# Performance work log

Measured on AMD Instinct MI355X. Metric: run time of the kernel, lower is better.

The kernel has to match this reference:

```python
import jax, jax.numpy as jnp
import numpy as np

N = 100_000      # nodes
E = 1_600_000    # edges
F_IN = 4         # num_features
H = 128          # hidden_channels
C = 5            # num_classes
G = 256          # graphs in batch


def setup_inputs() -> dict:
    key = jax.random.key(0)
    ks = jax.random.split(key, 14)
    x = jax.random.normal(ks[0], (N, F_IN), dtype=jnp.float32)
    edge_index = jax.random.randint(ks[1], (2, E), 0, N, dtype=jnp.int64)
    batch = jnp.sort(jax.random.randint(ks[2], (N,), 0, G, dtype=jnp.int64))
    def lin(k, fan_in, fan_out):
        kw, kb = jax.random.split(k)
        s = 1.0 / np.sqrt(fan_in)
        W = jax.random.uniform(kw, (fan_in, fan_out), jnp.float32, -s, s)
        b = jax.random.uniform(kb, (fan_out,), jnp.float32, -s, s)
        return W, b
    W1, b1 = lin(ks[3], F_IN, H)
    W2, b2 = lin(ks[4], H, H)
    W3, b3 = lin(ks[5], H, H)
    W4, b4 = lin(ks[6], H, H)
    Wl, bl = lin(ks[7], H, C)
    return {"x": x, "edge_index": edge_index, "batch": batch,
            "W1": W1, "b1": b1, "W2": W2, "b2": b2,
            "W3": W3, "b3": b3, "W4": W4, "b4": b4,
            "Wl": Wl, "bl": bl}


def reference(x, edge_index, batch, W1, b1, W2, b2, W3, b3, W4, b4, Wl, bl):
    n = x.shape[0]
    loop = jnp.arange(n, dtype=edge_index.dtype)
    src = jnp.concatenate([edge_index[0], loop])  # [E+N], with self-loops
    dst = jnp.concatenate([edge_index[1], loop])
    # symmetric normalization on A + I (PyG GCNConv default)
    deg = jax.ops.segment_sum(jnp.ones_like(dst, dtype=x.dtype), dst, num_segments=n)
    dinv = deg ** -0.5  # deg >= 1 thanks to self-loops
    coef = dinv[src] * dinv[dst]  # per-edge norm [E+N]

    def conv(h, W, b):
        h = h @ W                               # [N, H]
        msg = h[src] * coef[:, None]            # gather + scale [E+N, H]
        return jax.ops.segment_sum(msg, dst, num_segments=n) + b

    h = jax.nn.relu(conv(x, W1, b1))
    h = jax.nn.relu(conv(h, W2, b2))
    h = jax.nn.relu(conv(h, W3, b3))
    h = jax.nn.relu(conv(h, W4, b4))

    # global_mean_pool over graph ids
    counts = jax.ops.segment_sum(jnp.ones((n,), h.dtype), batch, num_segments=G)
    pooled = jax.ops.segment_sum(h, batch, num_segments=G)
    pooled = pooled / jnp.maximum(counts, 1.0)[:, None]  # [G, H]

    return jax.nn.sigmoid(pooled @ Wl + bl)  # [G, C]
```

## Files before the change

kernel.cpp:

```cpp
#include <hip/hip_runtime.h>
#include <hip/hip_fp8.h>
#include <math.h>

#define N_NODES 100000
#define N_EDGES 1600000
#define F_IN    4
#define HID     128
#define N_CLS   5
#define N_GRAPH 256
#define POOL_SEG 8

#define BSHIFT   9
#define BSIZE    512
#define NBUK     196
#define NCHUNK   200
#define CHUNK    8000

typedef _Float16 f16;
typedef _Float16 f16x2 __attribute__((ext_vector_type(2)));
typedef _Float16 f16x8 __attribute__((ext_vector_type(8)));
typedef float f32x4 __attribute__((ext_vector_type(4)));

__device__ __forceinline__ float rec_coef(unsigned r) {
    return (float)__builtin_bit_cast(_Float16, (unsigned short)(r & 0x7FFFu));
}

__device__ __forceinline__ float2 fp8x2_to_f32x2(unsigned short raw) {
    __hip_fp8x2_e4m3 t;
    t.__x = raw;
    return static_cast<float2>(t);
}

__device__ __forceinline__ void fma8(float c, uint2 v, float* acc) {
    float2 p0 = fp8x2_to_f32x2((unsigned short)(v.x & 0xFFFFu));
    float2 p1 = fp8x2_to_f32x2((unsigned short)(v.x >> 16));
    float2 p2 = fp8x2_to_f32x2((unsigned short)(v.y & 0xFFFFu));
    float2 p3 = fp8x2_to_f32x2((unsigned short)(v.y >> 16));
    acc[0] = fmaf(c, p0.x, acc[0]); acc[1] = fmaf(c, p0.y, acc[1]);
    acc[2] = fmaf(c, p1.x, acc[2]); acc[3] = fmaf(c, p1.y, acc[3]);
    acc[4] = fmaf(c, p2.x, acc[4]); acc[5] = fmaf(c, p2.y, acc[5]);
    acc[6] = fmaf(c, p3.x, acc[6]); acc[7] = fmaf(c, p3.y, acc[7]);
}

__global__ __launch_bounds__(256) void k_bc(const int* __restrict__ dst, int* __restrict__ C) {
    __shared__ int cnt[NBUK];
    int t = threadIdx.x;
    if (t < NBUK) cnt[t] = 0;
    __syncthreads();
    int base = blockIdx.x * CHUNK;
#pragma unroll
    for (int it = 0; it < 32; ++it) {
        int idx = it * 256 + t;
        if (idx < CHUNK) atomicAdd(&cnt[dst[base + idx] >> BSHIFT], 1);
    }
    __syncthreads();
    if (t < NBUK) C[blockIdx.x * NBUK + t] = cnt[t];
}

__global__ __launch_bounds__(256) void k_bscan(const int* __restrict__ C, int* __restrict__ Off,
                                               int* __restrict__ bbase) {
    __shared__ int s[256];
    int b = threadIdx.x;
    int tot = 0;
    if (b < NBUK) {
        for (int c = 0; c < NCHUNK; ++c) {
            Off[c * NBUK + b] = tot;
            tot += C[c * NBUK + b];
        }
    }
    s[b] = (b < NBUK) ? tot : 0;
    __syncthreads();
    for (int off = 1; off < 256; off <<= 1) {
        int v = (b >= off) ? s[b - off] : 0;
        __syncthreads();
        s[b] += v;
        __syncthreads();
    }
    if (b < NBUK) bbase[b] = s[b] - tot;
    if (b == 0) bbase[NBUK] = N_EDGES;
}

__global__ __launch_bounds__(256) void k_scatter(const int* __restrict__ src, const int* __restrict__ dst,
                                                 const int* __restrict__ Off, const int* __restrict__ bbase,
                                                 unsigned* __restrict__ bkt) {
    __shared__ int cur[NBUK];
    int t = threadIdx.x;
    if (t < NBUK) cur[t] = bbase[t] + Off[blockIdx.x * NBUK + t];
    __syncthreads();
    int base = blockIdx.x * CHUNK;
#pragma unroll
    for (int it = 0; it < 32; ++it) {
        int idx = it * 256 + t;
        if (idx < CHUNK) {
            int s = src[base + idx], d = dst[base + idx];
            int b = d >> BSHIFT;
            int p = atomicAdd(&cur[b], 1);
            bkt[p] = ((unsigned)s << BSHIFT) | (unsigned)(d & (BSIZE - 1));
        }
    }
}

__global__ __launch_bounds__(256) void k_hist2(const unsigned* __restrict__ bkt,
                                               const int* __restrict__ bbase,
                                               int* __restrict__ deg, float* __restrict__ dinv,
                                               int* __restrict__ padTot) {
    __shared__ int hist[BSIZE];
    __shared__ int tot;
    int t = threadIdx.x, b = blockIdx.x;
    hist[t] = 0; hist[t + 256] = 0;
    if (t == 0) tot = 0;
    __syncthreads();
    int s0 = bbase[b], s1 = bbase[b + 1];
    for (int e = s0 + t; e < s1; e += 256) atomicAdd(&hist[bkt[e] & (BSIZE - 1)], 1);
    __syncthreads();
    int loc = 0;
#pragma unroll
    for (int h = 0; h < 2; ++h) {
        int l = t + h * 256;
        int node = b * BSIZE + l;
        int d = hist[l];
        if (node < N_NODES) {
            deg[node] = d;
            dinv[node] = rsqrtf((float)d + 1.0f);
        }
        loc += (d + 15) >> 4;
    }
    atomicAdd(&tot, loc);
    __syncthreads();
    if (t == 0) padTot[b] = tot << 4;
}

__global__ __launch_bounds__(256) void k_pscan(const int* __restrict__ padTot, int* __restrict__ padBase,
                                               int* __restrict__ rowptrP) {
    __shared__ int s[256];
    int b = threadIdx.x;
    int v = (b < NBUK) ? padTot[b] : 0;
    s[b] = v;
    __syncthreads();
    for (int off = 1; off < 256; off <<= 1) {
        int u = (b >= off) ? s[b - off] : 0;
        __syncthreads();
        s[b] += u;
        __syncthreads();
    }
    if (b < NBUK) padBase[b] = s[b] - v;
    if (b == 0) {
        padBase[NBUK] = s[NBUK - 1];
        rowptrP[N_NODES] = s[NBUK - 1];
    }
}

__global__ __launch_bounds__(256) void k_local2(const unsigned* __restrict__ bkt,
                                                const int* __restrict__ bbase,
                                                const int* __restrict__ deg,
                                                const float* __restrict__ dinv,
                                                const int* __restrict__ padBase,
                                                int* __restrict__ rowptrP,
                                                unsigned* __restrict__ edges) {
    __shared__ int sc[BSIZE];
    __shared__ int cur[BSIZE];
    __shared__ float dv[BSIZE];
    int t = threadIdx.x, b = blockIdx.x;
    int base = padBase[b];
    int n0 = b * BSIZE + t, n1 = n0 + 256;
    int d0 = (n0 < N_NODES) ? deg[n0] : 0;
    int d1 = (n1 < N_NODES) ? deg[n1] : 0;
    int p0 = ((d0 + 15) >> 4) << 4;
    int p1 = ((d1 + 15) >> 4) << 4;
    sc[t] = p0; sc[t + 256] = p1;
    dv[t] = (n0 < N_NODES) ? dinv[n0] : 0.f;
    dv[t + 256] = (n1 < N_NODES) ? dinv[n1] : 0.f;
    __syncthreads();
    for (int off = 1; off < BSIZE; off <<= 1) {
        int i0 = t, i1 = t + 256;
        int v0 = (i0 >= off) ? sc[i0 - off] : 0;
        int v1 = (i1 >= off) ? sc[i1 - off] : 0;
        __syncthreads();
        sc[i0] += v0; sc[i1] += v1;
        __syncthreads();
    }
    int off0 = base + sc[t] - p0;
    int off1 = base + sc[t + 256] - p1;
    if (n0 < N_NODES) rowptrP[n0] = off0;
    if (n1 < N_NODES) rowptrP[n1] = off1;
    cur[t] = off0; cur[t + 256] = off1;
    int padT = sc[BSIZE - 1];
    for (int i = base + t; i < base + padT; i += 256) edges[i] = 0;
    __syncthreads();
    int s0 = bbase[b], s1 = bbase[b + 1];
    for (int e = s0 + t; e < s1; e += 256) {
        unsigned r = bkt[e];
        int dl = (int)(r & (BSIZE - 1));
        int s = (int)(r >> BSHIFT);
        int p = atomicAdd(&cur[dl], 1);
        float c = dv[dl] * dinv[s];
        unsigned short cb = __builtin_bit_cast(unsigned short, (f16)c);
        edges[p] = ((unsigned)s << 15) | (unsigned)(cb & 0x7FFFu);
    }
}

__global__ __launch_bounds__(256) void k_aggx1(const float4* __restrict__ x,
                                               const int* __restrict__ rowptrP,
                                               const unsigned* __restrict__ edges,
                                               const float* __restrict__ dinv,
                                               const float* __restrict__ W1, const float* __restrict__ b1,
                                               unsigned* __restrict__ hA) {
    __shared__ float4 sxa[16];
    __shared__ float sW[4 * HID];
    __shared__ float sb[HID];
    int t = threadIdx.x;
    sW[t] = W1[t];
    sW[t + 256] = W1[t + 256];
    if (t < HID) sb[t] = b1[t];
    int grp = t >> 4;
    int l = t & 15;
    int node = blockIdx.x * 16 + grp;
    int beg = rowptrP[node], end = rowptrP[node + 1];
    float ax = 0.f, ay = 0.f, az = 0.f, aw = 0.f;
    for (int e = beg + l; e < end; e += 16) {
        unsigned r = edges[e];
        float c = rec_coef(r);
        float4 v = x[r >> 15];
        ax = fmaf(c, v.x, ax); ay = fmaf(c, v.y, ay);
        az = fmaf(c, v.z, az); aw = fmaf(c, v.w, aw);
    }
#pragma unroll
    for (int off = 1; off < 16; off <<= 1) {
        ax += __shfl_xor(ax, off, 64);
        ay += __shfl_xor(ay, off, 64);
        az += __shfl_xor(az, off, 64);
        aw += __shfl_xor(aw, off, 64);
    }
    if (l == 0) {
        float di = dinv[node];
        float c0 = di * di;
        float4 xv = x[node];
        sxa[grp] = make_float4(fmaf(c0, xv.x, ax), fmaf(c0, xv.y, ay),
                               fmaf(c0, xv.z, az), fmaf(c0, xv.w, aw));
    }
    __syncthreads();

    int node0 = blockIdx.x * 16;
#pragma unroll
    for (int it = 0; it < 2; ++it) {
        int id = it * 256 + t;
        int n = id >> 5;
        int g = id & 31;
        float4 a = sxa[n];
        float c[4];
#pragma unroll
        for (int j = 0; j < 4; ++j) {
            int col = g * 4 + j;
            float v = sb[col];
            v = fmaf(a.x, sW[col],           v);
            v = fmaf(a.y, sW[HID + col],     v);
            v = fmaf(a.z, sW[2 * HID + col], v);
            v = fmaf(a.w, sW[3 * HID + col], v);
            c[j] = fmaxf(v, 0.0f);
        }
        unsigned lo = __hip_fp8x2_e4m3(make_float2(c[0], c[1])).__x;
        unsigned hi = __hip_fp8x2_e4m3(make_float2(c[2], c[3])).__x;
        hA[(node0 + n) * 32 + g] = lo | (hi << 16);
    }
}

template <bool FP8OUT>
__global__ __launch_bounds__(1024, 8) void k_aggemm8(const unsigned* __restrict__ h8,
                                                     const int* __restrict__ rowptrP,
                                                     const unsigned* __restrict__ edges,
                                                     const float* __restrict__ dinv,
                                                     const f16* __restrict__ Wp,
                                                     const float* __restrict__ bias,
                                                     void* __restrict__ outv) {
    __shared__ f16 S[16 * HID];
    int wave = threadIdx.x >> 6;
    int lane = threadIdx.x & 63;
    int node0 = blockIdx.x * 16;
    int node = node0 + wave;
    int g = lane >> 4;
    int l = lane & 15;
    int beg = rowptrP[node], end = rowptrP[node + 1];
    const char* hp = (const char*)h8 + l * 8;

    float acc[8];
    {
        float di = dinv[node];
        float c0 = (g == 0) ? di * di : 0.0f;
        uint2 v = *(const uint2*)(hp + ((size_t)node << 7));
        float2 p0 = fp8x2_to_f32x2((unsigned short)(v.x & 0xFFFFu));
        float2 p1 = fp8x2_to_f32x2((unsigned short)(v.x >> 16));
        float2 p2 = fp8x2_to_f32x2((unsigned short)(v.y & 0xFFFFu));
        float2 p3 = fp8x2_to_f32x2((unsigned short)(v.y >> 16));
        acc[0] = c0 * p0.x; acc[1] = c0 * p0.y;
        acc[2] = c0 * p1.x; acc[3] = c0 * p1.y;
        acc[4] = c0 * p2.x; acc[5] = c0 * p2.y;
        acc[6] = c0 * p3.x; acc[7] = c0 * p3.y;
    }

    for (int e = beg; e < end; e += 16) {
        unsigned rec16 = edges[e + l];
#pragma unroll
        for (int i = 0; i < 4; ++i) {
            unsigned rec = __shfl(rec16, i * 4 + g, 64);
            float c = rec_coef(rec);
            uint2 v = *(const uint2*)(hp + ((rec >> 8) & 0xFFFFFF80u));
            fma8(c, v, acc);
        }
    }

#pragma unroll
    for (int j = 0; j < 8; ++j) {
        acc[j] += __shfl_xor(acc[j], 16, 64);
        acc[j] += __shfl_xor(acc[j], 32, 64);
    }
    if (lane < 16) {
        f16x8 o;
#pragma unroll
        for (int j = 0; j < 8; ++j) o[j] = (f16)acc[j];
        int dw = (l * 4) ^ ((wave & 7) << 2);
        *(f16x8*)&S[wave * HID + dw * 2] = o;
    }
    __syncthreads();

    if (wave < 8) {
        int t = wave;
        int m = lane & 15;
        int q = lane >> 4;
        f32x4 c4 = (f32x4){0.f, 0.f, 0.f, 0.f};
#pragma unroll
        for (int ks = 0; ks < 4; ++ks) {
            int dw = (ks * 16 + q * 4) ^ ((m & 7) << 2);
            f16x8 a = *(const f16x8*)&S[m * HID + dw * 2];
            f16x8 b = *(const f16x8*)(Wp + ((size_t)(t * 4 + ks) * 64 + lane) * 8);
            c4 = __builtin_amdgcn_mfma_f32_16x16x32_f16(a, b, c4, 0, 0, 0);
        }
        float bb = bias[t * 16 + m];
#pragma unroll
        for (int r = 0; r < 4; ++r) {
            float val = fmaxf(c4[r] + bb, 0.0f);
            int row = node0 + q * 4 + r;
            if constexpr (FP8OUT) {
                ((__hip_fp8_e4m3*)outv)[(size_t)row * HID + t * 16 + m] = __hip_fp8_e4m3(val);
            } else {
                ((f16*)outv)[(size_t)row * HID + t * 16 + m] = (f16)val;
            }
        }
    }
}

__global__ __launch_bounds__(256) void k_packW3(const float* __restrict__ W2, const float* __restrict__ W3,
                                                const float* __restrict__ W4, f16* __restrict__ Wp) {
    int idx = blockIdx.x * 256 + threadIdx.x;
    int which = idx >> 14;
    int r = idx & 16383;
    const float* W = (which == 0) ? W2 : (which == 1) ? W3 : W4;
    int j  = r & 7;
    int L  = (r >> 3) & 63;
    int ks = (r >> 9) & 3;
    int ct = r >> 11;
    int k = ks * 32 + (L >> 4) * 8 + j;
    int n = ct * 16 + (L & 15);
    Wp[idx] = (f16)W[k * HID + n];
}

__device__ __forceinline__ int lower_bound_batch(const int* __restrict__ batch, int val) {
    int lo = 0, hi = N_NODES;
    while (lo < hi) { int m = (lo + hi) >> 1; if (batch[m] < val) lo = m + 1; else hi = m; }
    return lo;
}

__global__ __launch_bounds__(128) void k_pool1(const f16* __restrict__ h, const int* __restrict__ batch,
                                               float* __restrict__ partials) {
    int g = blockIdx.x / POOL_SEG;
    int s = blockIdx.x % POOL_SEG;
    int f = threadIdx.x;
    int beg = lower_bound_batch(batch, g);
    int end = lower_bound_batch(batch, g + 1);
    int len = end - beg;
    int sb = beg + (int)(((long long)len * s) / POOL_SEG);
    int se = beg + (int)(((long long)len * (s + 1)) / POOL_SEG);
    float acc = 0.0f;
    for (int i = sb; i < se; ++i) acc += (float)h[i * HID + f];
    partials[(size_t)blockIdx.x * HID + f] = acc;
}

__global__ __launch_bounds__(128) void k_pool2h(const float* __restrict__ partials,
                                                const int* __restrict__ batch,
                                                const float* __restrict__ Wl, const float* __restrict__ bl,
                                                float* __restrict__ out) {
    __shared__ float sp[HID];
    int g = blockIdx.x;
    int f = threadIdx.x;
    float acc = 0.0f;
#pragma unroll
    for (int s = 0; s < POOL_SEG; ++s)
        acc += partials[(size_t)(g * POOL_SEG + s) * HID + f];
    int beg = lower_bound_batch(batch, g);
    int end = lower_bound_batch(batch, g + 1);
    sp[f] = acc / fmaxf((float)(end - beg), 1.0f);
    __syncthreads();
    if (f < N_CLS) {
        float v = bl[f];
        for (int k = 0; k < HID; ++k) v = fmaf(sp[k], Wl[k * N_CLS + f], v);
        out[g * N_CLS + f] = 1.0f / (1.0f + expf(-v));
    }
}

extern "C" void kernel_launch(void* const* d_in, const int* in_sizes, int n_in,
                              void* d_out, int out_size, void* d_ws, size_t ws_size,
                              hipStream_t stream) {
    const float* x     = (const float*)d_in[0];
    const int*   ei    = (const int*)d_in[1];
    const int*   batch = (const int*)d_in[2];
    const float* W1 = (const float*)d_in[3];  const float* b1 = (const float*)d_in[4];
    const float* W2 = (const float*)d_in[5];  const float* b2 = (const float*)d_in[6];
    const float* W3 = (const float*)d_in[7];  const float* b3 = (const float*)d_in[8];
    const float* W4 = (const float*)d_in[9];  const float* b4 = (const float*)d_in[10];
    const float* Wl = (const float*)d_in[11]; const float* bl = (const float*)d_in[12];
    float* out = (float*)d_out;

    const size_t EPAD = (size_t)N_EDGES + (size_t)N_NODES * 16;

    char* p = (char*)d_ws;
    auto alloc = [&](size_t bytes) { char* r = p; p += (bytes + 255) & ~(size_t)255; return (void*)r; };
    int*      C       = (int*)     alloc((size_t)NCHUNK * NBUK * 4);
    int*      Off     = (int*)     alloc((size_t)NCHUNK * NBUK * 4);
    int*      bbase   = (int*)     alloc((size_t)(NBUK + 1) * 4);
    int*      padTot  = (int*)     alloc((size_t)NBUK * 4);
    int*      padBase = (int*)     alloc((size_t)(NBUK + 1) * 4);
    unsigned* bkt     = (unsigned*)alloc((size_t)N_EDGES * 4);
    int*      deg     = (int*)     alloc((size_t)N_NODES * 4);
    int*      rowptrP = (int*)     alloc((size_t)(N_NODES + 1) * 4);
    float*    dinv    = (float*)   alloc((size_t)N_NODES * 4);
    unsigned* edges   = (unsigned*)alloc(EPAD * 4);
    unsigned* hA      = (unsigned*)alloc((size_t)N_NODES * HID);
    unsigned* hC      = (unsigned*)alloc((size_t)N_NODES * HID);
    f16*      h4      = (f16*)     alloc((size_t)N_NODES * HID * 2);
    float*    parts   = (float*)   alloc((size_t)N_GRAPH * POOL_SEG * HID * 4);
    f16*      Wp      = (f16*)     alloc((size_t)3 * HID * HID * 2);
    f16*      Wp2 = Wp;
    f16*      Wp3 = Wp + HID * HID;
    f16*      Wp4 = Wp + 2 * HID * HID;

    const int* srcv = ei;
    const int* dstv = ei + N_EDGES;

    k_bc     <<<NCHUNK, 256, 0, stream>>>(dstv, C);
    k_bscan  <<<1, 256, 0, stream>>>(C, Off, bbase);
    k_scatter<<<NCHUNK, 256, 0, stream>>>(srcv, dstv, Off, bbase, bkt);
    k_hist2  <<<NBUK, 256, 0, stream>>>(bkt, bbase, deg, dinv, padTot);
    k_pscan  <<<1, 256, 0, stream>>>(padTot, padBase, rowptrP);
    k_local2 <<<NBUK, 256, 0, stream>>>(bkt, bbase, deg, dinv, padBase, rowptrP, edges);

    k_packW3<<<192, 256, 0, stream>>>(W2, W3, W4, Wp);

    k_aggx1<<<N_NODES / 16, 256, 0, stream>>>((const float4*)x, rowptrP, edges, dinv, W1, b1, hA);

    const int fgrid = N_NODES / 16;
    k_aggemm8<true ><<<fgrid, 1024, 0, stream>>>(hA, rowptrP, edges, dinv, Wp2, b2, hC);
    k_aggemm8<true ><<<fgrid, 1024, 0, stream>>>(hC, rowptrP, edges, dinv, Wp3, b3, hA);
    k_aggemm8<false><<<fgrid, 1024, 0, stream>>>(hA, rowptrP, edges, dinv, Wp4, b4, h4);

    k_pool1 <<<N_GRAPH * POOL_SEG, 128, 0, stream>>>(h4, batch, parts);
    k_pool2h<<<N_GRAPH, 128, 0, stream>>>(parts, batch, Wl, bl, out);
}
```

Before: 359.1 us.

## Use packed fp16 accumulation and 4-edge padding in fp8 aggregation kernel

The gather-aggregate kernel now accumulates in packed f16x2 using a direct fp8-to-f16 conversion builtin, halving accumulator registers and FMA count. Per-node edge padding shrinks from 16 to 4, so less padded work is done. Edge records are loaded directly per lane group with guarded loads instead of a shuffle. Row bounds are made wave-uniform with readfirstlane. Accumulating in fp16 risks precision loss on high-degree nodes, and the guarded loads add branches.

Measured after the change: 382.3 us. 6.5% more time.

```diff
diff --git a/kernel.cpp b/kernel.cpp
--- a/kernel.cpp
+++ b/kernel.cpp
@@ -25,21 +25,39 @@
     return (float)__builtin_bit_cast(_Float16, (unsigned short)(r & 0x7FFFu));
 }
 
+__device__ __forceinline__ f16x2 rec_coef2(unsigned r) {
+    unsigned c = r & 0x7FFFu;
+    return __builtin_bit_cast(f16x2, (c << 16) | c);
+}
+
 __device__ __forceinline__ float2 fp8x2_to_f32x2(unsigned short raw) {
     __hip_fp8x2_e4m3 t;
     t.__x = raw;
     return static_cast<float2>(t);
 }
 
-__device__ __forceinline__ void fma8(float c, uint2 v, float* acc) {
-    float2 p0 = fp8x2_to_f32x2((unsigned short)(v.x & 0xFFFFu));
-    float2 p1 = fp8x2_to_f32x2((unsigned short)(v.x >> 16));
-    float2 p2 = fp8x2_to_f32x2((unsigned short)(v.y & 0xFFFFu));
-    float2 p3 = fp8x2_to_f32x2((unsigned short)(v.y >> 16));
-    acc[0] = fmaf(c, p0.x, acc[0]); acc[1] = fmaf(c, p0.y, acc[1]);
-    acc[2] = fmaf(c, p1.x, acc[2]); acc[3] = fmaf(c, p1.y, acc[3]);
-    acc[4] = fmaf(c, p2.x, acc[4]); acc[5] = fmaf(c, p2.y, acc[5]);
-    acc[6] = fmaf(c, p3.x, acc[6]); acc[7] = fmaf(c, p3.y, acc[7]);
+#if __has_builtin(__builtin_amdgcn_cvt_pk_f16_fp8)
+__device__ __forceinline__ f16x2 cvt_h2(unsigned v) {
+    auto t = __builtin_amdgcn_cvt_pk_f16_fp8((short)v);
+    return __builtin_bit_cast(f16x2, t);
+}
+#else
+__device__ __forceinline__ f16x2 cvt_h2(unsigned v) {
+    float2 f = fp8x2_to_f32x2((unsigned short)v);
+    auto t = __builtin_amdgcn_cvt_pkrtz(f.x, f.y);
+    return __builtin_bit_cast(f16x2, t);
+}
+#endif
+
+__device__ __forceinline__ void fma8h(f16x2 c2, uint2 v, f16x2* acc) {
+    acc[0] += c2 * cvt_h2(v.x);
+    acc[1] += c2 * cvt_h2(v.x >> 16);
+    acc[2] += c2 * cvt_h2(v.y);
+    acc[3] += c2 * cvt_h2(v.y >> 16);
+}
+
+__device__ __forceinline__ f16x2 shfl_xor_h2(f16x2 a, int m) {
+    return __builtin_bit_cast(f16x2, __shfl_xor(__builtin_bit_cast(int, a), m, 64));
 }
 
 __global__ __launch_bounds__(256) void k_bc(const int* __restrict__ dst, int* __restrict__ C) {
@@ -123,11 +141,11 @@
             deg[node] = d;
             dinv[node] = rsqrtf((float)d + 1.0f);
         }
-        loc += (d + 15) >> 4;
+        loc += (d + 3) >> 2;
     }
     atomicAdd(&tot, loc);
     __syncthreads();
-    if (t == 0) padTot[b] = tot << 4;
+    if (t == 0) padTot[b] = tot << 2;
 }
 
 __global__ __launch_bounds__(256) void k_pscan(const int* __restrict__ padTot, int* __restrict__ padBase,
@@ -165,8 +183,8 @@
     int n0 = b * BSIZE + t, n1 = n0 + 256;
     int d0 = (n0 < N_NODES) ? deg[n0] : 0;
     int d1 = (n1 < N_NODES) ? deg[n1] : 0;
-    int p0 = ((d0 + 15) >> 4) << 4;
-    int p1 = ((d1 + 15) >> 4) << 4;
+    int p0 = ((d0 + 3) >> 2) << 2;
+    int p1 = ((d1 + 3) >> 2) << 2;
     sc[t] = p0; sc[t + 256] = p1;
     dv[t] = (n0 < N_NODES) ? dinv[n0] : 0.f;
     dv[t + 256] = (n1 < N_NODES) ? dinv[n1] : 0.f;
@@ -279,44 +297,47 @@
     int node = node0 + wave;
     int g = lane >> 4;
     int l = lane & 15;
-    int beg = rowptrP[node], end = rowptrP[node + 1];
-    const char* hp = (const char*)h8 + l * 8;
-
-    float acc[8];
+    int beg = __builtin_amdgcn_readfirstlane(rowptrP[node]);
+    int end = __builtin_amdgcn_readfirstlane(rowptrP[node + 1]);
+    const char* h8c = (const char*)h8;
+    unsigned lo8 = (unsigned)(l * 8);
+
+    f16x2 acc[4];
+    acc[0] = (f16x2){0, 0}; acc[1] = (f16x2){0, 0};
+    acc[2] = (f16x2){0, 0}; acc[3] = (f16x2){0, 0};
     {
         float di = dinv[node];
-        float c0 = (g == 0) ? di * di : 0.0f;
-        uint2 v = *(const uint2*)(hp + ((size_t)node << 7));
-        float2 p0 = fp8x2_to_f32x2((unsigned short)(v.x & 0xFFFFu));
-        float2 p1 = fp8x2_to_f32x2((unsigned short)(v.x >> 16));
-        float2 p2 = fp8x2_to_f32x2((unsigned short)(v.y & 0xFFFFu));
-        float2 p3 = fp8x2_to_f32x2((unsigned short)(v.y >> 16));
-        acc[0] = c0 * p0.x; acc[1] = c0 * p0.y;
-        acc[2] = c0 * p1.x; acc[3] = c0 * p1.y;
-        acc[4] = c0 * p2.x; acc[5] = c0 * p2.y;
-        acc[6] = c0 * p3.x; acc[7] = c0 * p3.y;
+        f16x2 c02 = (f16x2){0, 0};
+        if (g == 0) { f16 c0 = (f16)(di * di); c02.x = c0; c02.y = c0; }
+        uint2 v = *(const uint2*)(h8c + ((((unsigned)node << 7)) | lo8));
+        fma8h(c02, v, acc);
     }
 
     for (int e = beg; e < end; e += 16) {
-        unsigned rec16 = edges[e + l];
-#pragma unroll
-        for (int i = 0; i < 4; ++i) {
-            unsigned rec = __shfl(rec16, i * 4 + g, 64);
-            float c = rec_coef(rec);
-            uint2 v = *(const uint2*)(hp + ((rec >> 8) & 0xFFFFFF80u));
-            fma8(c, v, acc);
-        }
-    }
-
-#pragma unroll
-    for (int j = 0; j < 8; ++j) {
-        acc[j] += __shfl_xor(acc[j], 16, 64);
-        acc[j] += __shfl_xor(acc[j], 32, 64);
+        unsigned r0 = edges[e + g];
+        unsigned r1 = 0, r2 = 0, r3 = 0;
+        if (e + 4  < end) r1 = edges[e + 4  + g];
+        if (e + 8  < end) r2 = edges[e + 8  + g];
+        if (e + 12 < end) r3 = edges[e + 12 + g];
+        uint2 v0 = *(const uint2*)(h8c + (((r0 >> 8) & 0xFFFFFF80u) | lo8));
+        uint2 v1 = *(const uint2*)(h8c + (((r1 >> 8) & 0xFFFFFF80u) | lo8));
+        uint2 v2 = *(const uint2*)(h8c + (((r2 >> 8) & 0xFFFFFF80u) | lo8));
+        uint2 v3 = *(const uint2*)(h8c + (((r3 >> 8) & 0xFFFFFF80u) | lo8));
+        fma8h(rec_coef2(r0), v0, acc);
+        fma8h(rec_coef2(r1), v1, acc);
+        fma8h(rec_coef2(r2), v2, acc);
+        fma8h(rec_coef2(r3), v3, acc);
+    }
+
+#pragma unroll
+    for (int j = 0; j < 4; ++j) {
+        acc[j] += shfl_xor_h2(acc[j], 16);
+        acc[j] += shfl_xor_h2(acc[j], 32);
     }
     if (lane < 16) {
         f16x8 o;
-#pragma unroll
-        for (int j = 0; j < 8; ++j) o[j] = (f16)acc[j];
+        o[0] = acc[0][0]; o[1] = acc[0][1]; o[2] = acc[1][0]; o[3] = acc[1][1];
+        o[4] = acc[2][0]; o[5] = acc[2][1]; o[6] = acc[3][0]; o[7] = acc[3][1];
         int dw = (l * 4) ^ ((wave & 7) << 2);
         *(f16x8*)&S[wave * HID + dw * 2] = o;
     }
```
